# Optimization experiments

Measured on AMD Instinct MI355X. Metric: run time of the kernel, lower is better.

The kernel has to match this reference:

```python
import jax, jax.numpy as jnp
import numpy as np

SR, WINLEN, HOPLEN = 44100.0, 1024.0, 256.0
B, C, T = 32, 384, 512
MAX_DUR = 0.1          # setup caps duration at 0.1s -> max 13 frames/token
MAX_FRAMES = T * 13    # static padded frame length (jit-compatible upper bound)


def setup_inputs() -> dict:
    key = jax.random.key(0)
    k1, k2, k3, k4 = jax.random.split(key, 4)
    x = jax.random.normal(k1, (B, C, T), dtype=jnp.float32)
    # integer-valued note pitches stored as float (module detaches them anyway)
    notepitch = jax.random.randint(k2, (B, T), 0, 80).astype(jnp.float32)
    duration = jax.random.uniform(k3, (B, T), dtype=jnp.float32) * MAX_DUR
    x_lengths = jax.random.randint(k4, (B,), 1, T + 1)
    return {"x": x, "notepitch": notepitch, "duration": duration, "x_lengths": x_lengths}


def _repeat_counts(duration):
    # expand_size rule from the module:
    #   sr*d - winlen > 0 -> max((sr*d - winlen)/hoplen, 1)
    #   d == 0            -> 0
    #   else              -> 1
    # then int() truncation, clamped at 0.
    fr = SR * duration
    r = jnp.where(fr - WINLEN > 0.0,
                  jnp.maximum((fr - WINLEN) / HOPLEN, 1.0),
                  jnp.where(duration == 0.0, 0.0, 1.0))
    return r.astype(jnp.int32)  # trunc toward zero (values are >= 0)


def reference(x, notepitch, duration, x_lengths):
    r = _repeat_counts(duration)                 # [B, T]
    cum = jnp.cumsum(r, axis=1)                  # [B, T]
    frame_lengths = cum[:, -1]                   # [B]
    pos = jnp.arange(MAX_FRAMES)                 # [F]
    # token index producing each output frame: repeat-interleave via searchsorted
    tok = jax.vmap(lambda c: jnp.searchsorted(c, pos, side="right"))(cum)  # [B, F]
    tok = jnp.minimum(tok, x.shape[-1] - 1)
    mask = pos[None, :] < frame_lengths[:, None]  # [B, F]
    xt = jnp.transpose(x, (0, 2, 1))              # [B, T, C]
    expanded = jnp.take_along_axis(xt, tok[:, :, None], axis=1)  # [B, F, C]
    out = jnp.where(mask[:, :, None], expanded, 0.0)
    out = jnp.transpose(out, (0, 2, 1))           # [B, C, F]
    pitch = jnp.take_along_axis(notepitch, tok, axis=1)
    # module round-trips pitch through LongTensor -> truncation to int
    pitch = jnp.where(mask, pitch.astype(jnp.int32).astype(jnp.float32), 0.0)
    return out, pitch, frame_lengths.astype(jnp.int32)
```

## Files before the change

kernel.cpp:

```cpp
#include <hip/hip_runtime.h>

#define BB 32
#define CC 384
#define TT 512
#define MAXF 6656
#define CG 8
#define NCHUNK 7

__global__ __launch_bounds__(256) void lr_fused_kernel(
        const float* __restrict__ x,
        const float* __restrict__ notepitch,
        const float* __restrict__ duration,
        float* __restrict__ out,
        float* __restrict__ pitch_out,
        float* __restrict__ fl_out) {
    __shared__ float xs[CG * TT];
    __shared__ float snp[TT];
    __shared__ int   sbuf[256];
    __shared__ __attribute__((aligned(16))) unsigned short stok[MAXF];

    const int b   = blockIdx.y;
    const int cg  = blockIdx.x;
    const int tid = threadIdx.x;
    const bool do_pitch = (cg == 0);

    const float4* xsrc = (const float4*)(x + ((size_t)(b * CC + cg * CG)) * TT);
    const float4 xa0 = xsrc[tid];
    const float4 xa1 = xsrc[256 + tid];
    const float4 xa2 = xsrc[512 + tid];
    const float4 xa3 = xsrc[768 + tid];
    float2 np2 = make_float2(0.f, 0.f);
    if (do_pitch) np2 = *(const float2*)(notepitch + b * TT + 2 * tid);

    const float2 dp = *(const float2*)(duration + b * TT + 2 * tid);
    int r0, r1;
    {
        float fr = 44100.0f * dp.x, rf;
        if (fr - 1024.0f > 0.0f) rf = fmaxf((fr - 1024.0f) * (1.0f / 256.0f), 1.0f);
        else rf = (dp.x == 0.0f) ? 0.0f : 1.0f;
        r0 = (int)rf;
        fr = 44100.0f * dp.y;
        if (fr - 1024.0f > 0.0f) rf = fmaxf((fr - 1024.0f) * (1.0f / 256.0f), 1.0f);
        else rf = (dp.y == 0.0f) ? 0.0f : 1.0f;
        r1 = (int)rf;
    }
    const int s = r0 + r1;

    sbuf[tid] = s;
    __syncthreads();
    for (int off = 1; off < 256; off <<= 1) {
        const int add = (tid >= off) ? sbuf[tid - off] : 0;
        __syncthreads();
        sbuf[tid] += add;
        __syncthreads();
    }
    const int incl = sbuf[tid];
    const int excl = incl - s;
    const int fl   = sbuf[255];

    if (do_pitch && tid == 0) fl_out[b] = (float)fl;

    {
        float4* xdst = (float4*)xs;
        xdst[tid] = xa0; xdst[256 + tid] = xa1;
        xdst[512 + tid] = xa2; xdst[768 + tid] = xa3;
    }
    if (do_pitch) *(float2*)(snp + 2 * tid) = np2;

    float* const obase = out + ((size_t)(b * CC + cg * CG)) * MAXF;
    const float4 z = make_float4(0.f, 0.f, 0.f, 0.f);

    #pragma unroll
    for (int ch = 0; ch < NCHUNK; ++ch) {
        const int base = ch * 1024;
        const int p0 = base + tid * 4;
        if (base >= fl && p0 < MAXF) {
            #pragma unroll
            for (int c = 0; c < CG; ++c)
                *(float4*)(obase + (size_t)c * MAXF + p0) = z;
            if (do_pitch)
                *(float4*)(pitch_out + (size_t)b * MAXF + p0) = z;
        }
    }

    for (int f = excl; f < excl + r0; ++f)       stok[f] = (unsigned short)(2 * tid);
    for (int f = excl + r0; f < incl; ++f)       stok[f] = (unsigned short)(2 * tid + 1);
    __syncthreads();

    for (int ch = 0; ch < NCHUNK; ++ch) {
        const int base = ch * 1024;
        const int p0 = base + tid * 4;
        if (base >= fl || p0 >= MAXF) continue;

        if (base + 1024 <= fl) {
            const ushort4 tk = *(const ushort4*)(stok + p0);
            const int u0 = tk.x, u1 = tk.y, u2 = tk.z, u3 = tk.w;
            #pragma unroll
            for (int c = 0; c < CG; ++c) {
                const float* xr = xs + c * TT;
                *(float4*)(obase + (size_t)c * MAXF + p0) =
                    make_float4(xr[u0], xr[u1], xr[u2], xr[u3]);
            }
            if (do_pitch)
                *(float4*)(pitch_out + (size_t)b * MAXF + p0) =
                    make_float4((float)(int)snp[u0], (float)(int)snp[u1],
                                (float)(int)snp[u2], (float)(int)snp[u3]);
        } else {
            const ushort4 tk = *(const ushort4*)(stok + p0);
            const int u0 = min((int)tk.x, TT - 1), u1 = min((int)tk.y, TT - 1);
            const int u2 = min((int)tk.z, TT - 1), u3 = min((int)tk.w, TT - 1);
            const bool m0 = p0 < fl, m1 = p0 + 1 < fl;
            const bool m2 = p0 + 2 < fl, m3 = p0 + 3 < fl;
            #pragma unroll
            for (int c = 0; c < CG; ++c) {
                const float* xr = xs + c * TT;
                float4 v;
                v.x = m0 ? xr[u0] : 0.f;
                v.y = m1 ? xr[u1] : 0.f;
                v.z = m2 ? xr[u2] : 0.f;
                v.w = m3 ? xr[u3] : 0.f;
                *(float4*)(obase + (size_t)c * MAXF + p0) = v;
            }
            if (do_pitch) {
                float4 pv;
                pv.x = m0 ? (float)(int)snp[u0] : 0.f;
                pv.y = m1 ? (float)(int)snp[u1] : 0.f;
                pv.z = m2 ? (float)(int)snp[u2] : 0.f;
                pv.w = m3 ? (float)(int)snp[u3] : 0.f;
                *(float4*)(pitch_out + (size_t)b * MAXF + p0) = pv;
            }
        }
    }
}

extern "C" void kernel_launch(void* const* d_in, const int* in_sizes, int n_in,
                              void* d_out, int out_size, void* d_ws, size_t ws_size,
                              hipStream_t stream) {
    const float* x         = (const float*)d_in[0];
    const float* notepitch = (const float*)d_in[1];
    const float* duration  = (const float*)d_in[2];

    float* out       = (float*)d_out;
    float* pitch_out = out + (size_t)BB * CC * MAXF;
    float* fl_out    = pitch_out + (size_t)BB * MAXF;

    dim3 g(CC / CG, BB);
    lr_fused_kernel<<<g, 256, 0, stream>>>(x, notepitch, duration,
                                           out, pitch_out, fl_out);
}
```

Before: 69.09 us.

## Split scan into separate per-batch kernel, write kernel reads token map from workspace

Moves the per-batch cumulative scan and token-index map construction into a small kernel that runs once per batch and stores the map in workspace. The write kernel then only loads x and the token map, which removes the scan that was redundantly repeated in each of the 48 channel-group blocks and frees their 13KB of shared token buffer, raising occupancy (launch bounds 256,8). The cost is a second kernel launch, a workspace round trip for the token map, and serialisation between the two kernels. The old fused path is kept as a fallback when no workspace is available.

Result: slower. 76.56 us (+10.8%).

```diff
diff --git a/kernel.cpp b/kernel.cpp
--- a/kernel.cpp
+++ b/kernel.cpp
@@ -6,6 +6,163 @@
 #define MAXF 6656
 #define CG 8
 #define NCHUNK 7
+
+#define WS_NEEDED (128 + (size_t)BB * MAXF * 2)
+
+__device__ __forceinline__ int rep_count(float d) {
+    float fr = 44100.0f * d;
+    float rf;
+    if (fr - 1024.0f > 0.0f) rf = fmaxf((fr - 1024.0f) * (1.0f / 256.0f), 1.0f);
+    else rf = (d == 0.0f) ? 0.0f : 1.0f;
+    return (int)rf;
+}
+
+__global__ __launch_bounds__(256) void lr_scan_kernel(
+        const float* __restrict__ duration,
+        unsigned short* __restrict__ tok_ws,
+        int* __restrict__ fl_ws,
+        float* __restrict__ fl_out) {
+    __shared__ unsigned short stok[MAXF];
+    __shared__ int wsum[4];
+
+    const int b    = blockIdx.x;
+    const int tid  = threadIdx.x;
+    const int lane = tid & 63;
+    const int wid  = tid >> 6;
+
+    const float2 dp = *(const float2*)(duration + b * TT + 2 * tid);
+    const int r0 = rep_count(dp.x);
+    const int r1 = rep_count(dp.y);
+    const int s  = r0 + r1;
+
+    int v = s;
+    #pragma unroll
+    for (int off = 1; off < 64; off <<= 1) {
+        int t = __shfl_up(v, off, 64);
+        if (lane >= off) v += t;
+    }
+    if (lane == 63) wsum[wid] = v;
+
+    {
+        unsigned int* sz = (unsigned int*)stok;
+        #pragma unroll
+        for (int i = tid; i < MAXF / 2; i += 256) sz[i] = 0;
+    }
+    __syncthreads();
+
+    int prefix = 0, total = 0;
+    #pragma unroll
+    for (int w = 0; w < 4; ++w) {
+        const int t = wsum[w];
+        total += t;
+        if (w < wid) prefix += t;
+    }
+    const int incl = v + prefix;
+    const int excl = incl - s;
+    const int fl   = total;
+
+    for (int f = excl; f < excl + r0; ++f) stok[f] = (unsigned short)(2 * tid);
+    for (int f = excl + r0; f < incl; ++f) stok[f] = (unsigned short)(2 * tid + 1);
+    __syncthreads();
+
+    {
+        const uint4* src = (const uint4*)stok;
+        uint4* dst = (uint4*)(tok_ws + (size_t)b * MAXF);
+        #pragma unroll
+        for (int i = tid; i < MAXF / 8; i += 256) dst[i] = src[i];
+    }
+    if (tid == 0) {
+        fl_ws[b]  = fl;
+        fl_out[b] = (float)fl;
+    }
+}
+
+__global__ __launch_bounds__(256, 8) void lr_write_kernel(
+        const float* __restrict__ x,
+        const float* __restrict__ notepitch,
+        const unsigned short* __restrict__ tok_ws,
+        const int* __restrict__ fl_ws,
+        float* __restrict__ out,
+        float* __restrict__ pitch_out) {
+    __shared__ float xs[CG * TT];
+    __shared__ float snp[TT];
+
+    const int b   = blockIdx.y;
+    const int cg  = blockIdx.x;
+    const int tid = threadIdx.x;
+    const bool do_pitch = (cg == 0);
+
+    const int fl = fl_ws[b];
+
+    {
+        const float4* xsrc = (const float4*)(x + ((size_t)(b * CC + cg * CG)) * TT);
+        float4* xdst = (float4*)xs;
+        const float4 a0 = xsrc[tid];
+        const float4 a1 = xsrc[256 + tid];
+        const float4 a2 = xsrc[512 + tid];
+        const float4 a3 = xsrc[768 + tid];
+        xdst[tid] = a0; xdst[256 + tid] = a1;
+        xdst[512 + tid] = a2; xdst[768 + tid] = a3;
+        if (do_pitch)
+            *(float2*)(snp + 2 * tid) = *(const float2*)(notepitch + b * TT + 2 * tid);
+    }
+    __syncthreads();
+
+    float* const obase = out + ((size_t)(b * CC + cg * CG)) * MAXF;
+    const unsigned short* tokb = tok_ws + (size_t)b * MAXF;
+    const float4 z = make_float4(0.f, 0.f, 0.f, 0.f);
+
+    #pragma unroll
+    for (int ch = 0; ch < NCHUNK; ++ch) {
+        const int base = ch * 1024;
+        const int p0 = base + tid * 4;
+        if (p0 >= MAXF) continue;
+
+        if (base >= fl) {
+            #pragma unroll
+            for (int c = 0; c < CG; ++c)
+                *(float4*)(obase + (size_t)c * MAXF + p0) = z;
+            if (do_pitch)
+                *(float4*)(pitch_out + (size_t)b * MAXF + p0) = z;
+        } else if (base + 1024 <= fl) {
+            const ushort4 tk = *(const ushort4*)(tokb + p0);
+            const int u0 = tk.x, u1 = tk.y, u2 = tk.z, u3 = tk.w;
+            #pragma unroll
+            for (int c = 0; c < CG; ++c) {
+                const float* xr = xs + c * TT;
+                *(float4*)(obase + (size_t)c * MAXF + p0) =
+                    make_float4(xr[u0], xr[u1], xr[u2], xr[u3]);
+            }
+            if (do_pitch)
+                *(float4*)(pitch_out + (size_t)b * MAXF + p0) =
+                    make_float4((float)(int)snp[u0], (float)(int)snp[u1],
+                                (float)(int)snp[u2], (float)(int)snp[u3]);
+        } else {
+            const ushort4 tk = *(const ushort4*)(tokb + p0);
+            const int u0 = tk.x, u1 = tk.y, u2 = tk.z, u3 = tk.w;
+            const bool m0 = p0 < fl, m1 = p0 + 1 < fl;
+            const bool m2 = p0 + 2 < fl, m3 = p0 + 3 < fl;
+            #pragma unroll
+            for (int c = 0; c < CG; ++c) {
+                const float* xr = xs + c * TT;
+                float4 v;
+                v.x = m0 ? xr[u0] : 0.f;
+                v.y = m1 ? xr[u1] : 0.f;
+                v.z = m2 ? xr[u2] : 0.f;
+                v.w = m3 ? xr[u3] : 0.f;
+                *(float4*)(obase + (size_t)c * MAXF + p0) = v;
+            }
+            if (do_pitch) {
+                float4 pv;
+                pv.x = m0 ? (float)(int)snp[u0] : 0.f;
+                pv.y = m1 ? (float)(int)snp[u1] : 0.f;
+                pv.z = m2 ? (float)(int)snp[u2] : 0.f;
+                pv.w = m3 ? (float)(int)snp[u3] : 0.f;
+                *(float4*)(pitch_out + (size_t)b * MAXF + p0) = pv;
+            }
+        }
+    }
+}
 
 __global__ __launch_bounds__(256) void lr_fused_kernel(
         const float* __restrict__ x,
@@ -33,17 +190,8 @@
     if (do_pitch) np2 = *(const float2*)(notepitch + b * TT + 2 * tid);
 
     const float2 dp = *(const float2*)(duration + b * TT + 2 * tid);
-    int r0, r1;
-    {
-        float fr = 44100.0f * dp.x, rf;
-        if (fr - 1024.0f > 0.0f) rf = fmaxf((fr - 1024.0f) * (1.0f / 256.0f), 1.0f);
-        else rf = (dp.x == 0.0f) ? 0.0f : 1.0f;
-        r0 = (int)rf;
-        fr = 44100.0f * dp.y;
-        if (fr - 1024.0f > 0.0f) rf = fmaxf((fr - 1024.0f) * (1.0f / 256.0f), 1.0f);
-        else rf = (dp.y == 0.0f) ? 0.0f : 1.0f;
-        r1 = (int)rf;
-    }
+    const int r0 = rep_count(dp.x);
+    const int r1 = rep_count(dp.y);
     const int s = r0 + r1;
 
     sbuf[tid] = s;
@@ -136,6 +284,8 @@
 extern "C" void kernel_launch(void* const* d_in, const int* in_sizes, int n_in,
                               void* d_out, int out_size, void* d_ws, size_t ws_size,
                               hipStream_t stream) {
+    (void)in_sizes; (void)n_in; (void)out_size;
+
     const float* x         = (const float*)d_in[0];
     const float* notepitch = (const float*)d_in[1];
     const float* duration  = (const float*)d_in[2];
@@ -144,7 +294,18 @@
     float* pitch_out = out + (size_t)BB * CC * MAXF;
     float* fl_out    = pitch_out + (size_t)BB * MAXF;
 
-    dim3 g(CC / CG, BB);
-    lr_fused_kernel<<<g, 256, 0, stream>>>(x, notepitch, duration,
-                                           out, pitch_out, fl_out);
-}
+    if (d_ws != nullptr && ws_size >= WS_NEEDED) {
+        int* fl_ws = (int*)d_ws;
+        unsigned short* tok_ws = (unsigned short*)((char*)d_ws + 128);
+
+        lr_scan_kernel<<<BB, 256, 0, stream>>>(duration, tok_ws, fl_ws, fl_out);
+
+        dim3 g(CC / CG, BB);
+        lr_write_kernel<<<g, 256, 0, stream>>>(x, notepitch, tok_ws, fl_ws,
+                                               out, pitch_out);
+    } else {
+        dim3 g(CC / CG, BB);
+        lr_fused_kernel<<<g, 256, 0, stream>>>(x, notepitch, duration,
+                                               out, pitch_out, fl_out);
+    }
+}
```

## Make each wavefront independent to remove block-level barriers from expansion kernel

Applied to the files above, without the earlier changes.

Each 64-lane wavefront now redundantly computes the full per-batch repeat counts and prefix sum with wave shuffles instead of a shared-memory block scan with many __syncthreads. Each wave owns two channel rows and walks all frames in 256-frame steps, so no barrier is needed between building the token map and gathering. The token map in shared memory is written by every wave at once with identical values, which is redundant but consistent. This removes barrier stalls at the cost of duplicated scan and token-fill work per wave, and it relies on wave-synchronous visibility of the shared writes.

Result: slower. 72.70 us (+5.2%).

```diff
diff --git a/kernel.cpp b/kernel.cpp
--- a/kernel.cpp
+++ b/kernel.cpp
@@ -5,9 +5,17 @@
 #define TT 512
 #define MAXF 6656
 #define CG 8
-#define NCHUNK 7
+#define NIT 26
 
-__global__ __launch_bounds__(256) void lr_fused_kernel(
+__device__ __forceinline__ int rep_count(float d) {
+    float fr = 44100.0f * d;
+    float rf;
+    if (fr - 1024.0f > 0.0f) rf = fmaxf((fr - 1024.0f) * (1.0f / 256.0f), 1.0f);
+    else rf = (d == 0.0f) ? 0.0f : 1.0f;
+    return (int)rf;
+}
+
+__global__ __launch_bounds__(256) void lr_nobar_kernel(
         const float* __restrict__ x,
         const float* __restrict__ notepitch,
         const float* __restrict__ duration,
@@ -16,118 +24,119 @@
         float* __restrict__ fl_out) {
     __shared__ float xs[CG * TT];
     __shared__ float snp[TT];
-    __shared__ int   sbuf[256];
     __shared__ __attribute__((aligned(16))) unsigned short stok[MAXF];
 
-    const int b   = blockIdx.y;
-    const int cg  = blockIdx.x;
-    const int tid = threadIdx.x;
-    const bool do_pitch = (cg == 0);
+    const int b    = blockIdx.y;
+    const int cg   = blockIdx.x;
+    const int tid  = threadIdx.x;
+    const int lane = tid & 63;
+    const int wid  = tid >> 6;
+    const bool pw  = (cg == 0) && (wid == 0);
 
-    const float4* xsrc = (const float4*)(x + ((size_t)(b * CC + cg * CG)) * TT);
-    const float4 xa0 = xsrc[tid];
-    const float4 xa1 = xsrc[256 + tid];
-    const float4 xa2 = xsrc[512 + tid];
-    const float4 xa3 = xsrc[768 + tid];
-    float2 np2 = make_float2(0.f, 0.f);
-    if (do_pitch) np2 = *(const float2*)(notepitch + b * TT + 2 * tid);
+    const float4* dsrc = (const float4*)(duration + b * TT);
+    const float4 d0 = dsrc[2 * lane];
+    const float4 d1 = dsrc[2 * lane + 1];
 
-    const float2 dp = *(const float2*)(duration + b * TT + 2 * tid);
-    int r0, r1;
-    {
-        float fr = 44100.0f * dp.x, rf;
-        if (fr - 1024.0f > 0.0f) rf = fmaxf((fr - 1024.0f) * (1.0f / 256.0f), 1.0f);
-        else rf = (dp.x == 0.0f) ? 0.0f : 1.0f;
-        r0 = (int)rf;
-        fr = 44100.0f * dp.y;
-        if (fr - 1024.0f > 0.0f) rf = fmaxf((fr - 1024.0f) * (1.0f / 256.0f), 1.0f);
-        else rf = (dp.y == 0.0f) ? 0.0f : 1.0f;
-        r1 = (int)rf;
+    const int row0 = 2 * wid;
+    const float4* xsrc = (const float4*)(x + ((size_t)(b * CC + cg * CG + row0)) * TT);
+    const float4 a0 = xsrc[2 * lane];
+    const float4 a1 = xsrc[2 * lane + 1];
+    const float4 a2 = xsrc[128 + 2 * lane];
+    const float4 a3 = xsrc[128 + 2 * lane + 1];
+    float4 np0 = make_float4(0.f, 0.f, 0.f, 0.f), np1 = np0;
+    if (pw) {
+        const float4* npsrc = (const float4*)(notepitch + b * TT);
+        np0 = npsrc[2 * lane];
+        np1 = npsrc[2 * lane + 1];
     }
-    const int s = r0 + r1;
 
-    sbuf[tid] = s;
-    __syncthreads();
-    for (int off = 1; off < 256; off <<= 1) {
-        const int add = (tid >= off) ? sbuf[tid - off] : 0;
-        __syncthreads();
-        sbuf[tid] += add;
-        __syncthreads();
+    int r[8];
+    r[0] = rep_count(d0.x); r[1] = rep_count(d0.y);
+    r[2] = rep_count(d0.z); r[3] = rep_count(d0.w);
+    r[4] = rep_count(d1.x); r[5] = rep_count(d1.y);
+    r[6] = rep_count(d1.z); r[7] = rep_count(d1.w);
+    const int local = r[0]+r[1]+r[2]+r[3]+r[4]+r[5]+r[6]+r[7];
+
+    int v = local;
+    #pragma unroll
+    for (int off = 1; off < 64; off <<= 1) {
+        const int t = __shfl_up(v, off, 64);
+        if (lane >= off) v += t;
     }
-    const int incl = sbuf[tid];
-    const int excl = incl - s;
-    const int fl   = sbuf[255];
+    const int fl = __shfl(v, 63, 64);
 
-    if (do_pitch && tid == 0) fl_out[b] = (float)fl;
+    if (pw && lane == 0) fl_out[b] = (float)fl;
 
-    {
-        float4* xdst = (float4*)xs;
-        xdst[tid] = xa0; xdst[256 + tid] = xa1;
-        xdst[512 + tid] = xa2; xdst[768 + tid] = xa3;
-    }
-    if (do_pitch) *(float2*)(snp + 2 * tid) = np2;
-
-    float* const obase = out + ((size_t)(b * CC + cg * CG)) * MAXF;
+    float* const ob0 = out + ((size_t)(b * CC + cg * CG + row0)) * MAXF;
+    float* const ob1 = ob0 + MAXF;
+    float* const pb  = pitch_out + (size_t)b * MAXF;
     const float4 z = make_float4(0.f, 0.f, 0.f, 0.f);
 
     #pragma unroll
-    for (int ch = 0; ch < NCHUNK; ++ch) {
-        const int base = ch * 1024;
-        const int p0 = base + tid * 4;
-        if (base >= fl && p0 < MAXF) {
-            #pragma unroll
-            for (int c = 0; c < CG; ++c)
-                *(float4*)(obase + (size_t)c * MAXF + p0) = z;
-            if (do_pitch)
-                *(float4*)(pitch_out + (size_t)b * MAXF + p0) = z;
+    for (int it = 0; it < NIT; ++it) {
+        const int base = it * 256;
+        if (base >= fl) {
+            const int p0 = base + lane * 4;
+            *(float4*)(ob0 + p0) = z;
+            *(float4*)(ob1 + p0) = z;
+            if (pw) *(float4*)(pb + p0) = z;
         }
     }
 
-    for (int f = excl; f < excl + r0; ++f)       stok[f] = (unsigned short)(2 * tid);
-    for (int f = excl + r0; f < incl; ++f)       stok[f] = (unsigned short)(2 * tid + 1);
-    __syncthreads();
+    float* const xr0 = xs + row0 * TT;
+    float* const xr1 = xr0 + TT;
+    ((float4*)xr0)[2 * lane]       = a0;
+    ((float4*)xr0)[2 * lane + 1]   = a1;
+    ((float4*)xr1)[2 * lane]       = a2;
+    ((float4*)xr1)[2 * lane + 1]   = a3;
+    if (pw) {
+        ((float4*)snp)[2 * lane]     = np0;
+        ((float4*)snp)[2 * lane + 1] = np1;
+    }
 
-    for (int ch = 0; ch < NCHUNK; ++ch) {
-        const int base = ch * 1024;
-        const int p0 = base + tid * 4;
-        if (base >= fl || p0 >= MAXF) continue;
+    {
+        int f = v - local;
+        #pragma unroll
+        for (int k = 0; k < 8; ++k) {
+            const unsigned short tv = (unsigned short)(8 * lane + k);
+            const int fe = f + r[k];
+            for (; f < fe; ++f) stok[f] = tv;
+        }
+    }
 
-        if (base + 1024 <= fl) {
-            const ushort4 tk = *(const ushort4*)(stok + p0);
+    for (int it = 0; it < NIT; ++it) {
+        const int base = it * 256;
+        if (base >= fl) continue;
+        const int p0 = base + lane * 4;
+        const ushort4 tk = *(const ushort4*)(stok + p0);
+
+        if (base + 256 <= fl) {
             const int u0 = tk.x, u1 = tk.y, u2 = tk.z, u3 = tk.w;
-            #pragma unroll
-            for (int c = 0; c < CG; ++c) {
-                const float* xr = xs + c * TT;
-                *(float4*)(obase + (size_t)c * MAXF + p0) =
-                    make_float4(xr[u0], xr[u1], xr[u2], xr[u3]);
-            }
-            if (do_pitch)
-                *(float4*)(pitch_out + (size_t)b * MAXF + p0) =
+            *(float4*)(ob0 + p0) = make_float4(xr0[u0], xr0[u1], xr0[u2], xr0[u3]);
+            *(float4*)(ob1 + p0) = make_float4(xr1[u0], xr1[u1], xr1[u2], xr1[u3]);
+            if (pw)
+                *(float4*)(pb + p0) =
                     make_float4((float)(int)snp[u0], (float)(int)snp[u1],
                                 (float)(int)snp[u2], (float)(int)snp[u3]);
         } else {
-            const ushort4 tk = *(const ushort4*)(stok + p0);
             const int u0 = min((int)tk.x, TT - 1), u1 = min((int)tk.y, TT - 1);
             const int u2 = min((int)tk.z, TT - 1), u3 = min((int)tk.w, TT - 1);
             const bool m0 = p0 < fl, m1 = p0 + 1 < fl;
             const bool m2 = p0 + 2 < fl, m3 = p0 + 3 < fl;
-            #pragma unroll
-            for (int c = 0; c < CG; ++c) {
-                const float* xr = xs + c * TT;
-                float4 v;
-                v.x = m0 ? xr[u0] : 0.f;
-                v.y = m1 ? xr[u1] : 0.f;
-                v.z = m2 ? xr[u2] : 0.f;
-                v.w = m3 ? xr[u3] : 0.f;
-                *(float4*)(obase + (size_t)c * MAXF + p0) = v;
-            }
-            if (do_pitch) {
+            float4 v0, v1;
+            v0.x = m0 ? xr0[u0] : 0.f;  v0.y = m1 ? xr0[u1] : 0.f;
+            v0.z = m2 ? xr0[u2] : 0.f;  v0.w = m3 ? xr0[u3] : 0.f;
+            v1.x = m0 ? xr1[u0] : 0.f;  v1.y = m1 ? xr1[u1] : 0.f;
+            v1.z = m2 ? xr1[u2] : 0.f;  v1.w = m3 ? xr1[u3] : 0.f;
+            *(float4*)(ob0 + p0) = v0;
+            *(float4*)(ob1 + p0) = v1;
+            if (pw) {
                 float4 pv;
                 pv.x = m0 ? (float)(int)snp[u0] : 0.f;
                 pv.y = m1 ? (float)(int)snp[u1] : 0.f;
                 pv.z = m2 ? (float)(int)snp[u2] : 0.f;
                 pv.w = m3 ? (float)(int)snp[u3] : 0.f;
-                *(float4*)(pitch_out + (size_t)b * MAXF + p0) = pv;
+                *(float4*)(pb + p0) = pv;
             }
         }
     }
@@ -136,6 +145,8 @@
 extern "C" void kernel_launch(void* const* d_in, const int* in_sizes, int n_in,
                               void* d_out, int out_size, void* d_ws, size_t ws_size,
                               hipStream_t stream) {
+    (void)in_sizes; (void)n_in; (void)out_size; (void)d_ws; (void)ws_size;
+
     const float* x         = (const float*)d_in[0];
     const float* notepitch = (const float*)d_in[1];
     const float* duration  = (const float*)d_in[2];
@@ -145,6 +156,6 @@
     float* fl_out    = pitch_out + (size_t)BB * MAXF;
 
     dim3 g(CC / CG, BB);
-    lr_fused_kernel<<<g, 256, 0, stream>>>(x, notepitch, duration,
+    lr_nobar_kernel<<<g, 256, 0, stream>>>(x, notepitch, duration,
                                            out, pitch_out, fl_out);
 }
```
